# Optimization experiments

Measured on AMD Instinct MI355X. Metric: run time of the kernel, lower is better.

## Reference

```python
import jax, jax.numpy as jnp
import numpy as np
from math import sqrt

D_MODEL = 768
N_HEADS = 12
D_K = 64
D_V = 64
LN_EPS = 1e-5
NEG = -1e9


def layer_norm(x, g, b):
    mu = jnp.mean(x, axis=-1, keepdims=True)
    var = jnp.mean((x - mu) ** 2, axis=-1, keepdims=True)
    return (x - mu) * jax.lax.rsqrt(var + LN_EPS) * g + b


def setup_inputs() -> dict:
    key = jax.random.key(0)
    ks = jax.random.split(key, 8)
    B, S = 4, 1024
    pro1 = jax.random.normal(ks[0], (B, S, D_MODEL), dtype=jnp.float32)
    pro2 = jax.random.normal(ks[1], (B, S, D_MODEL), dtype=jnp.float32)
    # attn_mask is [B, H, S2, S1]; transpose(2,3) masks scores [B,H,S1,S2]
    mask1_2 = jax.random.bernoulli(ks[2], 0.3, (B, N_HEADS, S, S))
    sc = 1.0 / np.sqrt(D_MODEL)
    W_Q = jax.random.normal(ks[3], (D_MODEL, D_K * N_HEADS), dtype=jnp.float32) * sc
    W_K = jax.random.normal(ks[4], (D_MODEL, D_K * N_HEADS), dtype=jnp.float32) * sc
    fc1 = jax.random.normal(ks[5], (D_V * N_HEADS, D_MODEL), dtype=jnp.float32) * sc
    g1 = jnp.ones((D_MODEL,), jnp.float32)
    b1 = jnp.zeros((D_MODEL,), jnp.float32)
    g2 = jnp.ones((D_MODEL,), jnp.float32)
    b2 = jnp.zeros((D_MODEL,), jnp.float32)
    return {"pro1": pro1, "pro2": pro2, "mask1_2": mask1_2,
            "W_Q": W_Q, "W_K": W_K, "fc1": fc1,
            "g1": g1, "b1": b1, "g2": g2, "b2": b2}


def reference(pro1, pro2, mask1_2, W_Q, W_K, fc1, g1, b1, g2, b2):
    B, S1, _ = pro1.shape
    S2 = pro2.shape[1]
    # project and split heads: [B, H, S, d_k]
    Q = (pro1 @ W_Q).reshape(B, S1, N_HEADS, D_K).transpose(0, 2, 1, 3)
    K = (pro2 @ W_K).reshape(B, S2, N_HEADS, D_K).transpose(0, 2, 1, 3)
    scores = jnp.einsum('bhsd,bhtd->bhst', Q, K) / sqrt(D_K)  # [B,H,S1,S2]
    mask = jnp.swapaxes(mask1_2, 2, 3)  # attn_mask.transpose(2,3)
    scores = jnp.where(mask, NEG, scores)
    attn1 = jax.nn.softmax(scores, axis=-1)                  # over S2
    attn2 = jax.nn.softmax(jnp.swapaxes(scores, -1, -2), axis=-1)  # over S1
    ctx1 = jnp.einsum('bhst,bhtd->bhsd', attn1, K)  # [B,H,S1,d_k]
    ctx2 = jnp.einsum('bhts,bhsd->bhtd', attn2, Q)  # [B,H,S2,d_k]
    c1 = ctx1.transpose(0, 2, 1, 3).reshape(B, S1, N_HEADS * D_V)
    c2 = ctx2.transpose(0, 2, 1, 3).reshape(B, S2, N_HEADS * D_V)
    # NOTE: original applies fc1 to BOTH branches (fc2 is dead code)
    o1 = layer_norm(c1 @ fc1, g1, b1)
    o2 = layer_norm(c2 @ fc1, g2, b2)
    return (o1, o2)
```

## Files before the change

kernel.cpp:

```cpp
#include <hip/hip_runtime.h>
#include <hip/hip_bf16.h>
#include <stdint.h>

#define S 1024
#define DMODEL 768
#define NH 12
#define DK 64
#define BB 4
#define BH 48
#define M4 4096

typedef __attribute__((ext_vector_type(8))) short bf16x8;
typedef __attribute__((ext_vector_type(4))) float f32x4;
typedef __attribute__((ext_vector_type(4))) _Float16 f16x4;

static __device__ __forceinline__ unsigned short f2bf(float f) {
  unsigned int u = __float_as_uint(f);
  unsigned int r = u + 0x7FFFu + ((u >> 16) & 1u);
  return (unsigned short)(r >> 16);
}
static __device__ __forceinline__ unsigned int pk2(float a, float b) {
  return (unsigned int)f2bf(a) | ((unsigned int)f2bf(b) << 16);
}
static __device__ __forceinline__ bf16x8 ldfrag(const unsigned short* p) {
  uint4 q = *reinterpret_cast<const uint4*>(p);
  return __builtin_bit_cast(bf16x8, q);
}
static __device__ __forceinline__ unsigned short h2u(_Float16 h) {
  return __builtin_bit_cast(unsigned short, h);
}

__global__ __launch_bounds__(256) void k_transpose(const float* w0, const float* w1, const float* w2,
                                                   unsigned short* o0, unsigned short* o1, unsigned short* o2) {
  const float* in = blockIdx.z == 0 ? w0 : (blockIdx.z == 1 ? w1 : w2);
  unsigned short* out = blockIdx.z == 0 ? o0 : (blockIdx.z == 1 ? o1 : o2);
  __shared__ float tile[32][33];
  int n0 = blockIdx.x * 32, k0 = blockIdx.y * 32;
  int tid = threadIdx.x;
  int r = tid >> 3, c = (tid & 7) * 4;
  float4 v = *reinterpret_cast<const float4*>(in + (size_t)(k0 + r) * DMODEL + n0 + c);
  tile[r][c] = v.x; tile[r][c + 1] = v.y; tile[r][c + 2] = v.z; tile[r][c + 3] = v.w;
  __syncthreads();
  ushort4 o;
  o.x = f2bf(tile[c + 0][r]);
  o.y = f2bf(tile[c + 1][r]);
  o.z = f2bf(tile[c + 2][r]);
  o.w = f2bf(tile[c + 3][r]);
  *reinterpret_cast<ushort4*>(out + (size_t)(n0 + r) * DMODEL + k0 + c) = o;
}

__global__ __launch_bounds__(256) void k_pack(const int* __restrict__ mask,
                                              unsigned int* __restrict__ mp1,
                                              unsigned int* __restrict__ mp2) {
  int bh = blockIdx.y;
  int w = threadIdx.x >> 6, lane = threadIdx.x & 63;
  int tile = blockIdx.x * 4 + w;
  int ti = tile >> 4, tj = tile & 15;
  int t0 = ti * 64, s0 = tj * 64;
  const int* mb = mask + (size_t)bh * S * S;
  unsigned long long rowword = 0;
#pragma unroll 8
  for (int r = 0; r < 64; ++r) {
    int v = mb[(size_t)(t0 + r) * S + s0 + lane];
    unsigned long long b = __ballot(v != 0);
    if (lane == r) rowword = b;
  }
  unsigned int* p2 = mp2 + (size_t)bh * 32 * S;
  p2[((s0 >> 5) + 0) * S + t0 + lane] = (unsigned int)rowword;
  p2[((s0 >> 5) + 1) * S + t0 + lane] = (unsigned int)(rowword >> 32);
  unsigned long long colword = 0;
#pragma unroll
  for (int s = 0; s < 64; ++s) {
    unsigned long long b = __ballot((rowword >> s) & 1ull);
    if (lane == s) colword = b;
  }
  unsigned int* p1 = mp1 + (size_t)bh * 32 * S;
  p1[((t0 >> 5) + 0) * S + s0 + lane] = (unsigned int)colword;
  p1[((t0 >> 5) + 1) * S + s0 + lane] = (unsigned int)(colword >> 32);
}

__global__ __launch_bounds__(256, 2) void k_gemm128(
    int mode,
    const float* __restrict__ Af0, const float* __restrict__ Af1,
    const unsigned short* __restrict__ Ab0, const unsigned short* __restrict__ Ab1,
    const unsigned short* __restrict__ Bt0, const unsigned short* __restrict__ Bt1,
    unsigned short* __restrict__ oQ0, unsigned short* __restrict__ oQ1,
    unsigned short* __restrict__ oT0, unsigned short* __restrict__ oT1,
    float* __restrict__ oF0, float* __restrict__ oF1) {
  const float* Af = blockIdx.z ? Af1 : Af0;
  const unsigned short* Ab = blockIdx.z ? Ab1 : Ab0;
  const unsigned short* Bt = blockIdx.z ? Bt1 : Bt0;
  __shared__ __align__(16) unsigned short As[128 * 72];
  __shared__ __align__(16) unsigned short Bs[128 * 72];
  int tid = threadIdx.x;
  int m0 = blockIdx.x * 128, n0 = blockIdx.y * 128;
  int w = tid >> 6, lane = tid & 63, lane15 = lane & 15, quad = lane >> 4;
  int row0 = (w >> 1) * 64, col0 = (w & 1) * 64;
  f32x4 acc[4][4] = {};
  int sr = tid >> 2, sc = (tid & 3) * 16;
  const unsigned short* gB0 = Bt + (size_t)(n0 + sr) * DMODEL + sc;
  const unsigned short* gB1 = Bt + (size_t)(n0 + 64 + sr) * DMODEL + sc;
  uint4 vb[2][2];
  vb[0][0] = *reinterpret_cast<const uint4*>(gB0);
  vb[0][1] = *reinterpret_cast<const uint4*>(gB0 + 8);
  vb[1][0] = *reinterpret_cast<const uint4*>(gB1);
  vb[1][1] = *reinterpret_cast<const uint4*>(gB1 + 8);
  const float* gAf0 = Af + (size_t)(m0 + sr) * DMODEL + sc;
  const float* gAf1 = Af + (size_t)(m0 + 64 + sr) * DMODEL + sc;
  const unsigned short* gAb0 = Ab + (size_t)(m0 + sr) * DMODEL + sc;
  const unsigned short* gAb1 = Ab + (size_t)(m0 + 64 + sr) * DMODEL + sc;
  float4 fa[2][4];
  uint4 va[2][2];
  if (mode == 0) {
#pragma unroll
    for (int g = 0; g < 4; ++g) fa[0][g] = *reinterpret_cast<const float4*>(gAf0 + g * 4);
#pragma unroll
    for (int g = 0; g < 4; ++g) fa[1][g] = *reinterpret_cast<const float4*>(gAf1 + g * 4);
  } else {
    va[0][0] = *reinterpret_cast<const uint4*>(gAb0);
    va[0][1] = *reinterpret_cast<const uint4*>(gAb0 + 8);
    va[1][0] = *reinterpret_cast<const uint4*>(gAb1);
    va[1][1] = *reinterpret_cast<const uint4*>(gAb1 + 8);
  }
  for (int kc = 0; kc < 12; ++kc) {
    __syncthreads();
    if (mode == 0) {
#pragma unroll
      for (int h2 = 0; h2 < 2; ++h2) {
        uint4 u0, u1;
        u0.x = pk2(fa[h2][0].x, fa[h2][0].y); u0.y = pk2(fa[h2][0].z, fa[h2][0].w);
        u0.z = pk2(fa[h2][1].x, fa[h2][1].y); u0.w = pk2(fa[h2][1].z, fa[h2][1].w);
        u1.x = pk2(fa[h2][2].x, fa[h2][2].y); u1.y = pk2(fa[h2][2].z, fa[h2][2].w);
        u1.z = pk2(fa[h2][3].x, fa[h2][3].y); u1.w = pk2(fa[h2][3].z, fa[h2][3].w);
        *reinterpret_cast<uint4*>(&As[(h2 * 64 + sr) * 72 + sc]) = u0;
        *reinterpret_cast<uint4*>(&As[(h2 * 64 + sr) * 72 + sc + 8]) = u1;
      }
    } else {
#pragma unroll
      for (int h2 = 0; h2 < 2; ++h2) {
        *reinterpret_cast<uint4*>(&As[(h2 * 64 + sr) * 72 + sc]) = va[h2][0];
        *reinterpret_cast<uint4*>(&As[(h2 * 64 + sr) * 72 + sc + 8]) = va[h2][1];
      }
    }
#pragma unroll
    for (int h2 = 0; h2 < 2; ++h2) {
      *reinterpret_cast<uint4*>(&Bs[(h2 * 64 + sr) * 72 + sc]) = vb[h2][0];
      *reinterpret_cast<uint4*>(&Bs[(h2 * 64 + sr) * 72 + sc + 8]) = vb[h2][1];
    }
    if (kc < 11) {
      int k0 = (kc + 1) * 64;
      if (mode == 0) {
#pragma unroll
        for (int g = 0; g < 4; ++g) fa[0][g] = *reinterpret_cast<const float4*>(gAf0 + k0 + g * 4);
#pragma unroll
        for (int g = 0; g < 4; ++g) fa[1][g] = *reinterpret_cast<const float4*>(gAf1 + k0 + g * 4);
      } else {
        va[0][0] = *reinterpret_cast<const uint4*>(gAb0 + k0);
        va[0][1] = *reinterpret_cast<const uint4*>(gAb0 + k0 + 8);
        va[1][0] = *reinterpret_cast<const uint4*>(gAb1 + k0);
        va[1][1] = *reinterpret_cast<const uint4*>(gAb1 + k0 + 8);
      }
      vb[0][0] = *reinterpret_cast<const uint4*>(gB0 + k0);
      vb[0][1] = *reinterpret_cast<const uint4*>(gB0 + k0 + 8);
      vb[1][0] = *reinterpret_cast<const uint4*>(gB1 + k0);
      vb[1][1] = *reinterpret_cast<const uint4*>(gB1 + k0 + 8);
    }
    __syncthreads();
#pragma unroll
    for (int ks = 0; ks < 2; ++ks) {
      int kk = ks * 32 + quad * 8;
      bf16x8 a[4], b[4];
#pragma unroll
      for (int i = 0; i < 4; ++i) a[i] = ldfrag(&As[(row0 + i * 16 + lane15) * 72 + kk]);
#pragma unroll
      for (int j = 0; j < 4; ++j) b[j] = ldfrag(&Bs[(col0 + j * 16 + lane15) * 72 + kk]);
#pragma unroll
      for (int i = 0; i < 4; ++i)
#pragma unroll
        for (int j = 0; j < 4; ++j)
          acc[i][j] = __builtin_amdgcn_mfma_f32_16x16x32_bf16(a[i], b[j], acc[i][j], 0, 0, 0);
    }
  }
  if (mode == 0) {
    unsigned short* out = blockIdx.z ? oQ1 : oQ0;
    unsigned short* outT = blockIdx.z ? oT1 : oT0;
    f16x4 iden;
#pragma unroll
    for (int i = 0; i < 4; ++i) iden[i] = (_Float16)((quad * 4 + i) == lane15 ? 1.0f : 0.0f);
    f32x4 zero4 = {};
#pragma unroll
    for (int i = 0; i < 4; ++i)
#pragma unroll
      for (int j = 0; j < 4; ++j) {
#pragma unroll
        for (int reg = 0; reg < 4; ++reg) {
          int m = m0 + row0 + i * 16 + quad * 4 + reg;
          int n = n0 + col0 + j * 16 + lane15;
          int b = m >> 10, s = m & 1023, h = n >> 6, d = n & 63;
          out[(((size_t)(b * NH + h)) * S + s) * DK + d] = f2bf(acc[i][j][reg]);
        }
        f16x4 cf;
#pragma unroll
        for (int reg = 0; reg < 4; ++reg) cf[reg] = (_Float16)acc[i][j][reg];
        f32x4 tq = __builtin_amdgcn_mfma_f32_16x16x16f16(cf, iden, zero4, 0, 0, 0);
#pragma unroll
        for (int reg = 0; reg < 4; ++reg) {
          int n = n0 + col0 + j * 16 + quad * 4 + reg;
          int m = m0 + row0 + i * 16 + lane15;
          int b = m >> 10, s = m & 1023, h = n >> 6, d = n & 63;
          outT[(((size_t)(b * NH + h)) * DK + d) * S + s] = h2u((_Float16)tq[reg]);
        }
      }
  } else {
    float* out = blockIdx.z ? oF1 : oF0;
#pragma unroll
    for (int i = 0; i < 4; ++i)
#pragma unroll
      for (int j = 0; j < 4; ++j)
#pragma unroll
        for (int reg = 0; reg < 4; ++reg) {
          int m = m0 + row0 + i * 16 + quad * 4 + reg;
          int n = n0 + col0 + j * 16 + lane15;
          out[(size_t)m * DMODEL + n] = acc[i][j][reg];
        }
  }
}

__global__ __launch_bounds__(256, 3) void k_attn(
    const unsigned short* __restrict__ Qb, const unsigned short* __restrict__ Kb,
    const unsigned short* __restrict__ QT, const unsigned short* __restrict__ KT,
    const unsigned int* __restrict__ mp1, const unsigned int* __restrict__ mp2,
    unsigned short* __restrict__ c1, unsigned short* __restrict__ c2) {
  int bh = blockIdx.y, path = blockIdx.z;
  int s0b = blockIdx.x * 128;
  const unsigned short* X = path ? Kb : Qb;
  const unsigned short* Y = path ? Qb : Kb;
  const unsigned short* YT = path ? QT : KT;
  const unsigned int* mp = path ? mp2 : mp1;
  unsigned short* outc = path ? c2 : c1;

  __shared__ __align__(16) unsigned short YS[64 * 72];
  __shared__ __align__(16) unsigned short YTS[64 * 72];
  __shared__ unsigned int MW[128 * 33];

  const unsigned short* Xb = X + (size_t)bh * S * DK;
  const unsigned short* Yb = Y + (size_t)bh * S * DK;
  const unsigned short* YTb = YT + (size_t)bh * DK * S;
  const unsigned int* mb = mp + (size_t)bh * 32 * S;

  int tid = threadIdx.x;
  int w = tid >> 6, lane = tid & 63, lane15 = lane & 15, quad = lane >> 4;
  int s0w = s0b + w * 32;

  {
    int wd = tid >> 3, rb = (tid & 7) * 16;
#pragma unroll
    for (int u = 0; u < 4; ++u) {
      uint4 v = *reinterpret_cast<const uint4*>(mb + (size_t)wd * S + s0b + rb + u * 4);
      MW[(rb + u * 4 + 0) * 33 + wd] = v.x;
      MW[(rb + u * 4 + 1) * 33 + wd] = v.y;
      MW[(rb + u * 4 + 2) * 33 + wd] = v.z;
      MW[(rb + u * 4 + 3) * 33 + wd] = v.w;
    }
  }

  bf16x8 af[2][2];
#pragma unroll
  for (int rg = 0; rg < 2; ++rg) {
    af[rg][0] = ldfrag(Xb + (size_t)(s0w + rg * 16 + lane15) * DK + quad * 8);
    af[rg][1] = ldfrag(Xb + (size_t)(s0w + rg * 16 + lane15) * DK + 32 + quad * 8);
  }

  f16x4 iden;
#pragma unroll
  for (int i = 0; i < 4; ++i) iden[i] = (_Float16)((quad * 4 + i) == lane15 ? 1.0f : 0.0f);
  f32x4 zero4 = {};

  int sr4 = tid >> 2, sc4 = (tid & 3) * 16;
  const unsigned short* gY = Yb + (size_t)sr4 * DK + sc4;
  const unsigned short* gYT = YTb + (size_t)sr4 * S + sc4;
  uint4 y0 = *reinterpret_cast<const uint4*>(gY);
  uint4 y1 = *reinterpret_cast<const uint4*>(gY + 8);
  uint4 t0 = *reinterpret_cast<const uint4*>(gYT);
  uint4 t1 = *reinterpret_cast<const uint4*>(gYT + 8);

  f32x4 outa[2][4] = {};
  float lsum[2][4] = {};

  for (int jc = 0; jc < 16; ++jc) {
    __syncthreads();
    *reinterpret_cast<uint4*>(&YS[sr4 * 72 + sc4]) = y0;
    *reinterpret_cast<uint4*>(&YS[sr4 * 72 + sc4 + 8]) = y1;
    *reinterpret_cast<uint4*>(&YTS[sr4 * 72 + sc4]) = t0;
    *reinterpret_cast<uint4*>(&YTS[sr4 * 72 + sc4 + 8]) = t1;
    {
      int jn = (jc + 1 < 16) ? (jc + 1) * 64 : jc * 64;
      y0 = *reinterpret_cast<const uint4*>(gY + (size_t)jn * DK);
      y1 = *reinterpret_cast<const uint4*>(gY + (size_t)jn * DK + 8);
      t0 = *reinterpret_cast<const uint4*>(gYT + jn);
      t1 = *reinterpret_cast<const uint4*>(gYT + jn + 8);
    }
    __syncthreads();

    int j0 = jc * 64;
    int w0 = j0 >> 5;
    f32x4 sc[2][4];
#pragma unroll
    for (int st = 0; st < 4; ++st) {
      bf16x8 b0 = ldfrag(&YS[(st * 16 + lane15) * 72 + quad * 8]);
      bf16x8 b1 = ldfrag(&YS[(st * 16 + lane15) * 72 + 32 + quad * 8]);
#pragma unroll
      for (int rg = 0; rg < 2; ++rg) {
        f32x4 a = {};
        a = __builtin_amdgcn_mfma_f32_16x16x32_bf16(af[rg][0], b0, a, 0, 0, 0);
        a = __builtin_amdgcn_mfma_f32_16x16x32_bf16(af[rg][1], b1, a, 0, 0, 0);
        sc[rg][st] = a;
      }
    }
    f16x4 pfa[2][4];
#pragma unroll
    for (int rg = 0; rg < 2; ++rg) {
      unsigned int mw0[4], mw1[4];
#pragma unroll
      for (int reg = 0; reg < 4; ++reg) {
        int r = w * 32 + rg * 16 + quad * 4 + reg;
        mw0[reg] = MW[r * 33 + w0];
        mw1[reg] = MW[r * 33 + w0 + 1];
      }
#pragma unroll
      for (int st = 0; st < 4; ++st) {
        unsigned int sh = (unsigned)((st & 1) * 16 + lane15);
#pragma unroll
        for (int reg = 0; reg < 4; ++reg) {
          unsigned int wd = (st < 2) ? mw0[reg] : mw1[reg];
          float e = __expf(sc[rg][st][reg] * 0.125f);
          float p = ((wd >> sh) & 1u) ? 0.f : e;
          lsum[rg][reg] += p;
          pfa[rg][st][reg] = (_Float16)p;
        }
      }
    }
#pragma unroll
    for (int st = 0; st < 4; ++st) {
      f16x4 ptb[2];
#pragma unroll
      for (int rg = 0; rg < 2; ++rg) {
        f32x4 pt = __builtin_amdgcn_mfma_f32_16x16x16f16(pfa[rg][st], iden, zero4, 0, 0, 0);
        f16x4 pb;
#pragma unroll
        for (int i = 0; i < 4; ++i) pb[i] = (_Float16)pt[i];
        ptb[rg] = pb;
      }
#pragma unroll
      for (int dt = 0; dt < 4; ++dt) {
        uint2 q = *reinterpret_cast<const uint2*>(&YTS[(dt * 16 + lane15) * 72 + st * 16 + quad * 4]);
        f16x4 yb = __builtin_bit_cast(f16x4, q);
#pragma unroll
        for (int rg = 0; rg < 2; ++rg)
          outa[rg][dt] = __builtin_amdgcn_mfma_f32_16x16x16f16(ptb[rg], yb, outa[rg][dt], 0, 0, 0);
      }
    }
  }

#pragma unroll
  for (int rg = 0; rg < 2; ++rg)
#pragma unroll
    for (int reg = 0; reg < 4; ++reg) {
#pragma unroll
      for (int m = 1; m < 16; m <<= 1) lsum[rg][reg] += __shfl_xor(lsum[rg][reg], m);
      lsum[rg][reg] = 1.0f / lsum[rg][reg];
    }
  int b = bh / NH, h = bh % NH;
#pragma unroll
  for (int rg = 0; rg < 2; ++rg)
#pragma unroll
    for (int dt = 0; dt < 4; ++dt)
#pragma unroll
      for (int reg = 0; reg < 4; ++reg) {
        float v = outa[rg][dt][reg] * lsum[rg][reg];
        int srow = s0w + rg * 16 + quad * 4 + reg;
        size_t idx = ((size_t)(b * S) + srow) * DMODEL + h * DK + dt * 16 + lane15;
        outc[idx] = f2bf(v);
      }
}

__global__ __launch_bounds__(256) void k_ln(const float* __restrict__ f1, const float* __restrict__ f2,
                                            const float* __restrict__ g1, const float* __restrict__ b1,
                                            const float* __restrict__ g2, const float* __restrict__ b2,
                                            float* __restrict__ out) {
  int rowg = blockIdx.x;
  int sel = rowg >> 12;
  int row = rowg & 4095;
  const float* in = sel ? f2 : f1;
  const float* g = sel ? g2 : g1;
  const float* be = sel ? b2 : b1;
  int tid = threadIdx.x;
  const float* p = in + (size_t)row * DMODEL;
  float x0 = p[tid], x1 = p[tid + 256], x2 = p[tid + 512];
  float s = x0 + x1 + x2;
  float ss = x0 * x0 + x1 * x1 + x2 * x2;
#pragma unroll
  for (int m = 1; m < 64; m <<= 1) { s += __shfl_xor(s, m); ss += __shfl_xor(ss, m); }
  __shared__ float ps[4], pss[4];
  int w = tid >> 6;
  if ((tid & 63) == 0) { ps[w] = s; pss[w] = ss; }
  __syncthreads();
  s = ps[0] + ps[1] + ps[2] + ps[3];
  ss = pss[0] + pss[1] + pss[2] + pss[3];
  float mu = s * (1.0f / 768.0f);
  float var = ss * (1.0f / 768.0f) - mu * mu;
  float rstd = rsqrtf(var + 1e-5f);
  float* o = out + ((size_t)sel * M4 + row) * DMODEL;
  o[tid] = (x0 - mu) * rstd * g[tid] + be[tid];
  o[tid + 256] = (x1 - mu) * rstd * g[tid + 256] + be[tid + 256];
  o[tid + 512] = (x2 - mu) * rstd * g[tid + 512] + be[tid + 512];
}

extern "C" void kernel_launch(void* const* d_in, const int* in_sizes, int n_in,
                              void* d_out, int out_size, void* d_ws, size_t ws_size,
                              hipStream_t stream) {
  const float* pro1 = (const float*)d_in[0];
  const float* pro2 = (const float*)d_in[1];
  const int* mask = (const int*)d_in[2];
  const float* WQ = (const float*)d_in[3];
  const float* WK = (const float*)d_in[4];
  const float* FC1 = (const float*)d_in[5];
  const float* g1 = (const float*)d_in[6];
  const float* b1 = (const float*)d_in[7];
  const float* g2 = (const float*)d_in[8];
  const float* b2 = (const float*)d_in[9];
  float* out = (float*)d_out;
  char* ws = (char*)d_ws;

  float* f1 = (float*)(ws + 0);
  unsigned short* wqt = (unsigned short*)(ws + 12582912);
  unsigned short* wkt = (unsigned short*)(ws + 13762560);
  unsigned short* fc1t = (unsigned short*)(ws + 14942208);
  unsigned short* Qb = (unsigned short*)(ws + 16121856);
  unsigned short* Kb = (unsigned short*)(ws + 22413312);
  unsigned short* QT = (unsigned short*)(ws + 28704768);
  unsigned short* KT = (unsigned short*)(ws + 34996224);
  unsigned int* mp1 = (unsigned int*)(ws + 41287680);
  unsigned int* mp2 = (unsigned int*)(ws + 47579136);
  float* f2 = (float*)(ws + 41287680);
  unsigned short* c1 = (unsigned short*)(ws + 53870592);
  unsigned short* c2 = (unsigned short*)(ws + 60162048);

  k_transpose<<<dim3(24, 24, 3), 256, 0, stream>>>(WQ, WK, FC1, wqt, wkt, fc1t);
  k_pack<<<dim3(64, BH), 256, 0, stream>>>(mask, mp1, mp2);
  k_gemm128<<<dim3(32, 6, 2), 256, 0, stream>>>(0, pro1, pro2, nullptr, nullptr, wqt, wkt,
                                                Qb, Kb, QT, KT, nullptr, nullptr);
  k_attn<<<dim3(8, BH, 2), 256, 0, stream>>>(Qb, Kb, QT, KT, mp1, mp2, c1, c2);
  k_gemm128<<<dim3(32, 6, 2), 256, 0, stream>>>(1, nullptr, nullptr, c1, c2, fc1t, fc1t,
                                                nullptr, nullptr, nullptr, nullptr, f1, f2);
  k_ln<<<8192, 256, 0, stream>>>(f1, f2, g1, b1, g2, b2, out);
}
```

Measured before the change: 480.0 us.

## Compute transposed scores in attention to drop identity-MFMA transposes and mask copy

The attention kernel now computes S^T tiles by swapping MFMA operands, with Q/K stored as fp16. The P fragments can then feed the PV MFMA directly, without the identity-matrix transpose. The second packed-mask layout (mp1) and its ballot transpose in k_pack are removed, and both paths read the single packed mask through a small per-chunk prefetched shared buffer. The projection epilogue writes both the normal and transposed outputs as vectorized ushort4 stores, using the existing transpose MFMA, and both are now fp16 instead of bf16. This risks fp16 range and precision changes for Q/K, and a different mask indexing layout per path.

```diff
diff --git a/kernel.cpp b/kernel.cpp
--- a/kernel.cpp
+++ b/kernel.cpp
@@ -13,6 +13,7 @@
 typedef __attribute__((ext_vector_type(8))) short bf16x8;
 typedef __attribute__((ext_vector_type(4))) float f32x4;
 typedef __attribute__((ext_vector_type(4))) _Float16 f16x4;
+typedef __attribute__((ext_vector_type(8))) _Float16 f16x8;
 
 static __device__ __forceinline__ unsigned short f2bf(float f) {
   unsigned int u = __float_as_uint(f);
@@ -25,6 +26,10 @@
 static __device__ __forceinline__ bf16x8 ldfrag(const unsigned short* p) {
   uint4 q = *reinterpret_cast<const uint4*>(p);
   return __builtin_bit_cast(bf16x8, q);
+}
+static __device__ __forceinline__ f16x8 ldfragh(const unsigned short* p) {
+  uint4 q = *reinterpret_cast<const uint4*>(p);
+  return __builtin_bit_cast(f16x8, q);
 }
 static __device__ __forceinline__ unsigned short h2u(_Float16 h) {
   return __builtin_bit_cast(unsigned short, h);
@@ -50,7 +55,6 @@
 }
 
 __global__ __launch_bounds__(256) void k_pack(const int* __restrict__ mask,
-                                              unsigned int* __restrict__ mp1,
                                               unsigned int* __restrict__ mp2) {
   int bh = blockIdx.y;
   int w = threadIdx.x >> 6, lane = threadIdx.x & 63;
@@ -68,15 +72,6 @@
   unsigned int* p2 = mp2 + (size_t)bh * 32 * S;
   p2[((s0 >> 5) + 0) * S + t0 + lane] = (unsigned int)rowword;
   p2[((s0 >> 5) + 1) * S + t0 + lane] = (unsigned int)(rowword >> 32);
-  unsigned long long colword = 0;
-#pragma unroll
-  for (int s = 0; s < 64; ++s) {
-    unsigned long long b = __ballot((rowword >> s) & 1ull);
-    if (lane == s) colword = b;
-  }
-  unsigned int* p1 = mp1 + (size_t)bh * 32 * S;
-  p1[((t0 >> 5) + 0) * S + s0 + lane] = (unsigned int)colword;
-  p1[((t0 >> 5) + 1) * S + s0 + lane] = (unsigned int)(colword >> 32);
 }
 
 __global__ __launch_bounds__(256, 2) void k_gemm128(
@@ -192,23 +187,27 @@
     for (int i = 0; i < 4; ++i)
 #pragma unroll
       for (int j = 0; j < 4; ++j) {
-#pragma unroll
-        for (int reg = 0; reg < 4; ++reg) {
-          int m = m0 + row0 + i * 16 + quad * 4 + reg;
-          int n = n0 + col0 + j * 16 + lane15;
-          int b = m >> 10, s = m & 1023, h = n >> 6, d = n & 63;
-          out[(((size_t)(b * NH + h)) * S + s) * DK + d] = f2bf(acc[i][j][reg]);
-        }
         f16x4 cf;
 #pragma unroll
         for (int reg = 0; reg < 4; ++reg) cf[reg] = (_Float16)acc[i][j][reg];
         f32x4 tq = __builtin_amdgcn_mfma_f32_16x16x16f16(cf, iden, zero4, 0, 0, 0);
-#pragma unroll
-        for (int reg = 0; reg < 4; ++reg) {
-          int n = n0 + col0 + j * 16 + quad * 4 + reg;
+        {
           int m = m0 + row0 + i * 16 + lane15;
+          int n = n0 + col0 + j * 16 + quad * 4;
           int b = m >> 10, s = m & 1023, h = n >> 6, d = n & 63;
-          outT[(((size_t)(b * NH + h)) * DK + d) * S + s] = h2u((_Float16)tq[reg]);
+          ushort4 o;
+          o.x = h2u((_Float16)tq[0]); o.y = h2u((_Float16)tq[1]);
+          o.z = h2u((_Float16)tq[2]); o.w = h2u((_Float16)tq[3]);
+          *reinterpret_cast<ushort4*>(&out[(((size_t)(b * NH + h)) * S + s) * DK + d]) = o;
+        }
+        {
+          int n = n0 + col0 + j * 16 + lane15;
+          int m = m0 + row0 + i * 16 + quad * 4;
+          int b = m >> 10, s = m & 1023, h = n >> 6, d = n & 63;
+          ushort4 o;
+          o.x = h2u((_Float16)acc[i][j][0]); o.y = h2u((_Float16)acc[i][j][1]);
+          o.z = h2u((_Float16)acc[i][j][2]); o.w = h2u((_Float16)acc[i][j][3]);
+          *reinterpret_cast<ushort4*>(&outT[(((size_t)(b * NH + h)) * DK + d) * S + s]) = o;
         }
       }
   } else {
@@ -229,52 +228,34 @@
 __global__ __launch_bounds__(256, 3) void k_attn(
     const unsigned short* __restrict__ Qb, const unsigned short* __restrict__ Kb,
     const unsigned short* __restrict__ QT, const unsigned short* __restrict__ KT,
-    const unsigned int* __restrict__ mp1, const unsigned int* __restrict__ mp2,
+    const unsigned int* __restrict__ mp2,
     unsigned short* __restrict__ c1, unsigned short* __restrict__ c2) {
   int bh = blockIdx.y, path = blockIdx.z;
   int s0b = blockIdx.x * 128;
   const unsigned short* X = path ? Kb : Qb;
   const unsigned short* Y = path ? Qb : Kb;
   const unsigned short* YT = path ? QT : KT;
-  const unsigned int* mp = path ? mp2 : mp1;
   unsigned short* outc = path ? c2 : c1;
 
   __shared__ __align__(16) unsigned short YS[64 * 72];
   __shared__ __align__(16) unsigned short YTS[64 * 72];
-  __shared__ unsigned int MW[128 * 33];
+  __shared__ unsigned int MWS[256];
 
   const unsigned short* Xb = X + (size_t)bh * S * DK;
   const unsigned short* Yb = Y + (size_t)bh * S * DK;
   const unsigned short* YTb = YT + (size_t)bh * DK * S;
-  const unsigned int* mb = mp + (size_t)bh * 32 * S;
+  const unsigned int* mbg = mp2 + (size_t)bh * 32 * S;
 
   int tid = threadIdx.x;
   int w = tid >> 6, lane = tid & 63, lane15 = lane & 15, quad = lane >> 4;
   int s0w = s0b + w * 32;
 
-  {
-    int wd = tid >> 3, rb = (tid & 7) * 16;
-#pragma unroll
-    for (int u = 0; u < 4; ++u) {
-      uint4 v = *reinterpret_cast<const uint4*>(mb + (size_t)wd * S + s0b + rb + u * 4);
-      MW[(rb + u * 4 + 0) * 33 + wd] = v.x;
-      MW[(rb + u * 4 + 1) * 33 + wd] = v.y;
-      MW[(rb + u * 4 + 2) * 33 + wd] = v.z;
-      MW[(rb + u * 4 + 3) * 33 + wd] = v.w;
-    }
-  }
-
-  bf16x8 af[2][2];
+  f16x8 xf[2][2];
 #pragma unroll
   for (int rg = 0; rg < 2; ++rg) {
-    af[rg][0] = ldfrag(Xb + (size_t)(s0w + rg * 16 + lane15) * DK + quad * 8);
-    af[rg][1] = ldfrag(Xb + (size_t)(s0w + rg * 16 + lane15) * DK + 32 + quad * 8);
-  }
-
-  f16x4 iden;
-#pragma unroll
-  for (int i = 0; i < 4; ++i) iden[i] = (_Float16)((quad * 4 + i) == lane15 ? 1.0f : 0.0f);
-  f32x4 zero4 = {};
+    xf[rg][0] = ldfragh(Xb + (size_t)(s0w + rg * 16 + lane15) * DK + quad * 8);
+    xf[rg][1] = ldfragh(Xb + (size_t)(s0w + rg * 16 + lane15) * DK + 32 + quad * 8);
+  }
 
   int sr4 = tid >> 2, sc4 = (tid & 3) * 16;
   const unsigned short* gY = Yb + (size_t)sr4 * DK + sc4;
@@ -283,9 +264,13 @@
   uint4 y1 = *reinterpret_cast<const uint4*>(gY + 8);
   uint4 t0 = *reinterpret_cast<const uint4*>(gYT);
   uint4 t1 = *reinterpret_cast<const uint4*>(gYT + 8);
+  int mws_idx = (path == 0) ? ((tid & 63) * 4 + (tid >> 6)) : ((tid & 127) * 2 + (tid >> 7));
+  unsigned int mwv = (path == 0)
+      ? mbg[((size_t)((s0b >> 5) + (tid >> 6))) * S + (tid & 63)]
+      : mbg[((size_t)(tid >> 7)) * S + s0b + (tid & 127)];
 
   f32x4 outa[2][4] = {};
-  float lsum[2][4] = {};
+  float lsum[2] = {0.f, 0.f};
 
   for (int jc = 0; jc < 16; ++jc) {
     __syncthreads();
@@ -293,93 +278,100 @@
     *reinterpret_cast<uint4*>(&YS[sr4 * 72 + sc4 + 8]) = y1;
     *reinterpret_cast<uint4*>(&YTS[sr4 * 72 + sc4]) = t0;
     *reinterpret_cast<uint4*>(&YTS[sr4 * 72 + sc4 + 8]) = t1;
+    MWS[mws_idx] = mwv;
     {
       int jn = (jc + 1 < 16) ? (jc + 1) * 64 : jc * 64;
       y0 = *reinterpret_cast<const uint4*>(gY + (size_t)jn * DK);
       y1 = *reinterpret_cast<const uint4*>(gY + (size_t)jn * DK + 8);
       t0 = *reinterpret_cast<const uint4*>(gYT + jn);
       t1 = *reinterpret_cast<const uint4*>(gYT + jn + 8);
+      mwv = (path == 0)
+          ? mbg[((size_t)((s0b >> 5) + (tid >> 6))) * S + jn + (tid & 63)]
+          : mbg[((size_t)((jn >> 5) + (tid >> 7))) * S + s0b + (tid & 127)];
     }
     __syncthreads();
 
-    int j0 = jc * 64;
-    int w0 = j0 >> 5;
-    f32x4 sc[2][4];
+    f32x4 scv[4][2];
 #pragma unroll
     for (int st = 0; st < 4; ++st) {
-      bf16x8 b0 = ldfrag(&YS[(st * 16 + lane15) * 72 + quad * 8]);
-      bf16x8 b1 = ldfrag(&YS[(st * 16 + lane15) * 72 + 32 + quad * 8]);
+      f16x8 a0 = ldfragh(&YS[(st * 16 + lane15) * 72 + quad * 8]);
+      f16x8 a1 = ldfragh(&YS[(st * 16 + lane15) * 72 + 32 + quad * 8]);
 #pragma unroll
       for (int rg = 0; rg < 2; ++rg) {
-        f32x4 a = {};
-        a = __builtin_amdgcn_mfma_f32_16x16x32_bf16(af[rg][0], b0, a, 0, 0, 0);
-        a = __builtin_amdgcn_mfma_f32_16x16x32_bf16(af[rg][1], b1, a, 0, 0, 0);
-        sc[rg][st] = a;
-      }
-    }
-    f16x4 pfa[2][4];
-#pragma unroll
-    for (int rg = 0; rg < 2; ++rg) {
-      unsigned int mw0[4], mw1[4];
+        f32x4 v = {};
+        v = __builtin_amdgcn_mfma_f32_16x16x32_f16(a0, xf[rg][0], v, 0, 0, 0);
+        v = __builtin_amdgcn_mfma_f32_16x16x32_f16(a1, xf[rg][1], v, 0, 0, 0);
+        scv[st][rg] = v;
+      }
+    }
+    f16x4 pfa[4][2];
+    if (path == 0) {
+#pragma unroll
+      for (int st = 0; st < 4; ++st)
+#pragma unroll
+        for (int reg = 0; reg < 4; ++reg) {
+          unsigned int wdv = MWS[(st * 16 + quad * 4 + reg) * 4 + w];
+#pragma unroll
+          for (int rg = 0; rg < 2; ++rg) {
+            float e = __expf(scv[st][rg][reg] * 0.125f);
+            float p = ((wdv >> (unsigned)(rg * 16 + lane15)) & 1u) ? 0.f : e;
+            lsum[rg] += p;
+            pfa[st][rg][reg] = (_Float16)p;
+          }
+        }
+    } else {
+#pragma unroll
+      for (int rg = 0; rg < 2; ++rg) {
+        unsigned int wv0 = MWS[(w * 32 + rg * 16 + lane15) * 2 + 0];
+        unsigned int wv1 = MWS[(w * 32 + rg * 16 + lane15) * 2 + 1];
+#pragma unroll
+        for (int st = 0; st < 4; ++st) {
+          unsigned int wdv = (st < 2) ? wv0 : wv1;
+#pragma unroll
+          for (int reg = 0; reg < 4; ++reg) {
+            unsigned int sh = (unsigned)((st & 1) * 16 + quad * 4 + reg);
+            float e = __expf(scv[st][rg][reg] * 0.125f);
+            float p = ((wdv >> sh) & 1u) ? 0.f : e;
+            lsum[rg] += p;
+            pfa[st][rg][reg] = (_Float16)p;
+          }
+        }
+      }
+    }
+#pragma unroll
+    for (int st = 0; st < 4; ++st)
+#pragma unroll
+      for (int dsub = 0; dsub < 4; ++dsub) {
+        uint2 q = *reinterpret_cast<const uint2*>(&YTS[(dsub * 16 + lane15) * 72 + st * 16 + quad * 4]);
+        f16x4 yb = __builtin_bit_cast(f16x4, q);
+#pragma unroll
+        for (int rg = 0; rg < 2; ++rg)
+          outa[rg][dsub] = __builtin_amdgcn_mfma_f32_16x16x16f16(pfa[st][rg], yb, outa[rg][dsub], 0, 0, 0);
+      }
+  }
+
+#pragma unroll
+  for (int rg = 0; rg < 2; ++rg) {
+    lsum[rg] += __shfl_xor(lsum[rg], 16);
+    lsum[rg] += __shfl_xor(lsum[rg], 32);
+  }
+  float rinv[2][4];
+#pragma unroll
+  for (int rg = 0; rg < 2; ++rg)
+#pragma unroll
+    for (int reg = 0; reg < 4; ++reg)
+      rinv[rg][reg] = 1.0f / __shfl(lsum[rg], quad * 4 + reg);
+
+  int b = bh / NH, h = bh % NH;
+#pragma unroll
+  for (int rg = 0; rg < 2; ++rg)
+#pragma unroll
+    for (int dsub = 0; dsub < 4; ++dsub)
 #pragma unroll
       for (int reg = 0; reg < 4; ++reg) {
-        int r = w * 32 + rg * 16 + quad * 4 + reg;
-        mw0[reg] = MW[r * 33 + w0];
-        mw1[reg] = MW[r * 33 + w0 + 1];
-      }
-#pragma unroll
-      for (int st = 0; st < 4; ++st) {
-        unsigned int sh = (unsigned)((st & 1) * 16 + lane15);
-#pragma unroll
-        for (int reg = 0; reg < 4; ++reg) {
-          unsigned int wd = (st < 2) ? mw0[reg] : mw1[reg];
-          float e = __expf(sc[rg][st][reg] * 0.125f);
-          float p = ((wd >> sh) & 1u) ? 0.f : e;
-          lsum[rg][reg] += p;
-          pfa[rg][st][reg] = (_Float16)p;
-        }
-      }
-    }
-#pragma unroll
-    for (int st = 0; st < 4; ++st) {
-      f16x4 ptb[2];
-#pragma unroll
-      for (int rg = 0; rg < 2; ++rg) {
-        f32x4 pt = __builtin_amdgcn_mfma_f32_16x16x16f16(pfa[rg][st], iden, zero4, 0, 0, 0);
-        f16x4 pb;
-#pragma unroll
-        for (int i = 0; i < 4; ++i) pb[i] = (_Float16)pt[i];
-        ptb[rg] = pb;
-      }
-#pragma unroll
-      for (int dt = 0; dt < 4; ++dt) {
-        uint2 q = *reinterpret_cast<const uint2*>(&YTS[(dt * 16 + lane15) * 72 + st * 16 + quad * 4]);
-        f16x4 yb = __builtin_bit_cast(f16x4, q);
-#pragma unroll
-        for (int rg = 0; rg < 2; ++rg)
-          outa[rg][dt] = __builtin_amdgcn_mfma_f32_16x16x16f16(ptb[rg], yb, outa[rg][dt], 0, 0, 0);
-      }
-    }
-  }
-
-#pragma unroll
-  for (int rg = 0; rg < 2; ++rg)
-#pragma unroll
-    for (int reg = 0; reg < 4; ++reg) {
-#pragma unroll
-      for (int m = 1; m < 16; m <<= 1) lsum[rg][reg] += __shfl_xor(lsum[rg][reg], m);
-      lsum[rg][reg] = 1.0f / lsum[rg][reg];
-    }
-  int b = bh / NH, h = bh % NH;
-#pragma unroll
-  for (int rg = 0; rg < 2; ++rg)
-#pragma unroll
-    for (int dt = 0; dt < 4; ++dt)
-#pragma unroll
-      for (int reg = 0; reg < 4; ++reg) {
-        float v = outa[rg][dt][reg] * lsum[rg][reg];
+        float v = outa[rg][dsub][reg] * rinv[rg][reg];
         int srow = s0w + rg * 16 + quad * 4 + reg;
-        size_t idx = ((size_t)(b * S) + srow) * DMODEL + h * DK + dt * 16 + lane15;
+        size_t idx = ((size_t)(b * S) + srow) * DMODEL + h * DK + dsub * 16 + lane15;
         outc[idx] = f2bf(v);
       }
 }
@@ -440,17 +432,16 @@
   unsigned short* Kb = (unsigned short*)(ws + 22413312);
   unsigned short* QT = (unsigned short*)(ws + 28704768);
   unsigned short* KT = (unsigned short*)(ws + 34996224);
-  unsigned int* mp1 = (unsigned int*)(ws + 41287680);
-  unsigned int* mp2 = (unsigned int*)(ws + 47579136);
-  float* f2 = (float*)(ws + 41287680);
-  unsigned short* c1 = (unsigned short*)(ws + 53870592);
-  unsigned short* c2 = (unsigned short*)(ws + 60162048);
+  unsigned int* mp2 = (unsigned int*)(ws + 41287680);
+  float* f2 = (float*)(ws + 47579136);
+  unsigned short* c1 = (unsigned short*)(ws + 60162048);
+  unsigned short* c2 = (unsigned short*)(ws + 66453504);
 
   k_transpose<<<dim3(24, 24, 3), 256, 0, stream>>>(WQ, WK, FC1, wqt, wkt, fc1t);
-  k_pack<<<dim3(64, BH), 256, 0, stream>>>(mask, mp1, mp2);
+  k_pack<<<dim3(64, BH), 256, 0, stream>>>(mask, mp2);
   k_gemm128<<<dim3(32, 6, 2), 256, 0, stream>>>(0, pro1, pro2, nullptr, nullptr, wqt, wkt,
                                                 Qb, Kb, QT, KT, nullptr, nullptr);
-  k_attn<<<dim3(8, BH, 2), 256, 0, stream>>>(Qb, Kb, QT, KT, mp1, mp2, c1, c2);
+  k_attn<<<dim3(8, BH, 2), 256, 0, stream>>>(Qb, Kb, QT, KT, mp2, c1, c2);
   k_gemm128<<<dim3(32, 6, 2), 256, 0, stream>>>(1, nullptr, nullptr, c1, c2, fc1t, fc1t,
                                                 nullptr, nullptr, nullptr, nullptr, f1, f2);
   k_ln<<<8192, 256, 0, stream>>>(f1, f2, g1, b1, g2, b2, out);
```

Result: no change. 474.4 us (-1.2%).
